# Optimization experiments

Measured on AMD Instinct MI355X. Metric: run time of the kernel, lower is better.

The kernel has to match this reference:

```python
import jax, jax.numpy as jnp
import numpy as np

EPS = 1e-12

def _l2norm(v):
    # torch.nn.functional.normalize(p=2) with eps clamp
    return v / jnp.maximum(jnp.linalg.norm(v), EPS)

def _spectral_weight(W, U):
    # W: (out, in) flattened 1x1 conv weight; U: (1, out) power-iteration buffer.
    # One power iteration, all under stop_gradient (torch.no_grad in original).
    V = _l2norm(U @ W)            # (1, in)
    Unew = _l2norm(V @ W.T)       # (1, out)
    sigma = (Unew @ W @ V.T)[0, 0]
    return W / jax.lax.stop_gradient(sigma)

def _conv1x1(x, W, b):
    # x: (b,c,h,w), W: (o,c), b: (o,)
    return jnp.einsum('oc,bchw->bohw', W, x) + b[None, :, None, None]

def setup_inputs() -> dict:
    key = jax.random.key(0)
    ks = jax.random.split(key, 11)
    B, C, H, W = 4, 256, 64, 64
    Ck = C // 8
    return {
        'x':   jax.random.normal(ks[0], (B, C, H, W), jnp.float32),
        'f_w': jax.random.normal(ks[1], (Ck, C), jnp.float32) * 0.05,
        'f_b': jax.random.normal(ks[2], (Ck,), jnp.float32) * 0.05,
        'f_u': jax.random.uniform(ks[3], (1, Ck), jnp.float32),
        'g_w': jax.random.normal(ks[4], (Ck, C), jnp.float32) * 0.05,
        'g_b': jax.random.normal(ks[5], (Ck,), jnp.float32) * 0.05,
        'g_u': jax.random.uniform(ks[6], (1, Ck), jnp.float32),
        'h_w': jax.random.normal(ks[7], (C, C), jnp.float32) * 0.05,
        'h_b': jax.random.normal(ks[8], (C,), jnp.float32) * 0.05,
        'h_u': jax.random.uniform(ks[9], (1, C), jnp.float32),
        'gamma': jax.random.normal(ks[10], (1, 1), jnp.float32),
    }

def reference(x, f_w, f_b, f_u, g_w, g_b, g_u, h_w, h_b, h_u, gamma):
    b, c, h, w = x.shape
    hw = h * w
    key_ = _conv1x1(x, _spectral_weight(f_w, f_u), f_b).reshape(b, -1, hw).transpose(0, 2, 1)  # (b,hw,ck)
    query = _conv1x1(x, _spectral_weight(g_w, g_u), g_b).reshape(b, -1, hw)                    # (b,ck,hw)
    attn = jax.nn.softmax(jnp.einsum('bnd,bdm->bnm', key_, query), axis=-1)                    # (b,hw,hw)
    value = _conv1x1(x, _spectral_weight(h_w, h_u), h_b).reshape(b, -1, hw)                    # (b,c,hw)
    out = jnp.einsum('bnm,bcm->bnc', attn, value)                                              # (b,hw,c)
    # Faithful to original: raw view of (b,hw,c) contiguous buffer into (b,c,h,w)
    out = out.reshape(b, c, h, w)
    return gamma[0, 0] * out + x
```

## Files before the change

kernel.cpp:

```cpp
#include <hip/hip_runtime.h>


constexpr int kC   = 256;
constexpr int kHW  = 4096;
constexpr int kB   = 4;
constexpr int kCHW = kC * kHW;

typedef short bf16x8 __attribute__((ext_vector_type(8)));
typedef float f32x4  __attribute__((ext_vector_type(4)));
typedef unsigned short u16;

#if __has_builtin(__builtin_amdgcn_exp2f)
#define EXP2(x) __builtin_amdgcn_exp2f(x)
#else
#define EXP2(x) exp2f(x)
#endif

__device__ __forceinline__ u16 f2bf(float f) {
    union { float f; unsigned u; } v; v.f = f;
    unsigned u = v.u;
    return (u16)((u + 0x7fffu + ((u >> 16) & 1u)) >> 16);
}
__device__ __forceinline__ float bf2f(u16 h) {
    union { unsigned u; float f; } v; v.u = ((unsigned)h) << 16;
    return v.f;
}

__global__ __launch_bounds__(1024) void k_sigma(
    const float* __restrict__ fw, const float* __restrict__ fu,
    const float* __restrict__ gw, const float* __restrict__ gu,
    const float* __restrict__ hww, const float* __restrict__ hu,
    float* __restrict__ sig, u16* __restrict__ wh, u16* __restrict__ wl)
{
    const int which = blockIdx.x;
    const float* W = which == 0 ? fw : (which == 1 ? gw : hww);
    const float* U = which == 0 ? fu : (which == 1 ? gu : hu);
    const int O = (which == 2) ? 256 : 32;
    const int t = threadIdx.x;

    __shared__ float par[4][256];
    __shared__ float red[256];
    __shared__ __align__(16) float Vv[256];

    {
        const int i = t & 255, och = t >> 8;
        int olim = O - och * 64; olim = olim < 0 ? 0 : (olim > 64 ? 64 : olim);
        float p = 0.f;
        for (int oo = 0; oo < olim; ++oo) {
            const int o = och * 64 + oo;
            p += U[o] * W[o * 256 + i];
        }
        par[och][i] = p;
    }
    __syncthreads();
    float t1 = 0.f;
    if (t < 256) {
        t1 = par[0][t] + par[1][t] + par[2][t] + par[3][t];
        red[t] = t1 * t1;
    }
    __syncthreads();
    for (int s = 128; s > 0; s >>= 1) { if (t < s) red[t] += red[t + s]; __syncthreads(); }
    if (t < 256) Vv[t] = t1 / fmaxf(sqrtf(red[0]), 1e-12f);
    __syncthreads();

    {
        const int o = t & 255, ich = t >> 8;
        float q = 0.f;
        if (o < O) {
            const float4* Wr = (const float4*)(W + (size_t)o * 256 + ich * 64);
            const float4* Vr = (const float4*)(&Vv[ich * 64]);
#pragma unroll
            for (int j = 0; j < 16; ++j) {
                const float4 w = Wr[j]; const float4 v = Vr[j];
                q += w.x * v.x + w.y * v.y + w.z * v.z + w.w * v.w;
            }
        }
        par[ich][o] = q;
    }
    __syncthreads();
    if (t < 256) {
        const float t2 = par[0][t] + par[1][t] + par[2][t] + par[3][t];
        red[t] = t2 * t2;
    }
    __syncthreads();
    for (int s = 128; s > 0; s >>= 1) { if (t < s) red[t] += red[t + s]; __syncthreads(); }
    if (t == 0) {
        const float s2 = red[0];
        sig[which] = fmaxf(sqrtf(s2), 1e-12f) / s2;
    }

    const int nElem = O * 256;
    const int gbase = (which == 0) ? 0 : (which == 1 ? 32 : 64);
    for (int i = t; i < nElem; i += 1024) {
        const int o = i >> 8, ci = i & 255;
        const int g = gbase + o;
        const int idx = ((g >> 4) * 8 + (ci >> 5)) * 512 + (g & 15) * 32 + (ci & 31);
        const float f = W[i];
        const u16 h = f2bf(f);
        wh[idx] = h;
        wl[idx] = f2bf(f - bf2f(h));
    }
}

__global__ __launch_bounds__(512) void k_proj(
    const float* __restrict__ x,
    const u16* __restrict__ wh, const u16* __restrict__ wl,
    const float* __restrict__ fb, const float* __restrict__ gb,
    const float* __restrict__ hb, const float* __restrict__ sig,
    u16* __restrict__ Kc, u16* __restrict__ Qc, u16* __restrict__ Vb)
{
    __shared__ __align__(16) float xs[256][64];
    __shared__ float bLDS[320];

    const int t = threadIdx.x;
    const int wave = t >> 6, lane = t & 63;
    const int quad = lane >> 4, l15 = lane & 15;
    const int b = blockIdx.y;
    const int n0 = blockIdx.x * 64;
    const int nch = wave & 3, cohalf = wave >> 2;

    constexpr float kLog2e = 1.44269504f;

    {
        const int r4i = lane >> 4, c16 = lane & 15;
        const float* xg = x + (size_t)b * kCHW + (size_t)r4i * kHW + n0 + c16 * 4;
#pragma unroll
        for (int j = 0; j < 8; ++j) {
            const int cibase = (wave * 8 + j) * 4;
            __builtin_amdgcn_global_load_lds(
                (const __attribute__((address_space(1))) void*)(xg + (size_t)cibase * kHW),
                (__attribute__((address_space(3))) void*)&xs[cibase][0], 16, 0, 0);
        }
    }
    if (t < 320) bLDS[t] = (t < 32) ? fb[t]
                         : (t < 64) ? gb[t - 32] * kLog2e
                         : hb[t - 64];
    __syncthreads();

    const int n = nch * 16 + l15;
    bf16x8 bh[8], bl[8];
#pragma unroll
    for (int s = 0; s < 8; ++s) {
        union { u16 a[8]; bf16x8 v; } H, L;
#pragma unroll
        for (int j = 0; j < 8; ++j) {
            const float v = xs[s * 32 + quad * 8 + j][n];
            const u16 h = f2bf(v);
            H.a[j] = h; L.a[j] = f2bf(v - bf2f(h));
        }
        bh[s] = H.v; bl[s] = L.v;
    }

    const u16* whp = wh + l15 * 32 + quad * 8;
    const u16* wlp = wl + l15 * 32 + quad * 8;

    f32x4 acc[10] = {};
#pragma unroll
    for (int c = 0; c < 10; ++c) {
        const size_t base = (size_t)(cohalf * 10 + c) * 4096;
#pragma unroll
        for (int s = 0; s < 8; ++s) {
            const bf16x8 ah = *(const bf16x8*)(whp + base + s * 512);
            const bf16x8 al = *(const bf16x8*)(wlp + base + s * 512);
            acc[c] = __builtin_amdgcn_mfma_f32_16x16x32_bf16(ah, bh[s], acc[c], 0, 0, 0);
            acc[c] = __builtin_amdgcn_mfma_f32_16x16x32_bf16(ah, bl[s], acc[c], 0, 0, 0);
            acc[c] = __builtin_amdgcn_mfma_f32_16x16x32_bf16(al, bh[s], acc[c], 0, 0, 0);
        }
    }

    const float s0 = sig[0], s1 = sig[1] * kLog2e, s2 = sig[2];
#pragma unroll
    for (int c = 0; c < 10; ++c) {
        const int cog0 = (cohalf * 10 + c) * 16;
        const float inv = (cog0 < 32) ? s0 : (cog0 < 64) ? s1 : s2;
#pragma unroll
        for (int r = 0; r < 4; ++r) {
            const int co = cog0 + quad * 4 + r;
            const float v = acc[c][r] * inv + bLDS[co];
            if (co < 64) {
                u16* H = (co < 32) ? Kc : Qc;
                const int d = co & 31;
                const u16 h = f2bf(v);
                const u16 l = f2bf(v - bf2f(h));
                const size_t off = (size_t)(b * kHW + n0 + n) * 64;
                H[off + d] = h;
                H[off + 32 + d] = l;
            } else {
                Vb[((size_t)b * kC + (co - 64)) * kHW + n0 + n] = f2bf(v);
            }
        }
    }
}

__global__ __launch_bounds__(512, 4) void k_attn(
    const u16* __restrict__ Kc, const u16* __restrict__ Qc,
    const u16* __restrict__ Vb,
    u16* __restrict__ Op, float* __restrict__ Sl)
{
    __shared__ __align__(16) u16 Qt[2][4096];
    __shared__ __align__(16) u16 Pt[2][4096];
    __shared__ float lsum[8][16];

    const int t = threadIdx.x;
    const int wave = t >> 6, lane = t & 63;
    const int quad = lane >> 4, l15 = lane & 15;
    const int sg = wave >> 1, half = wave & 1;

    const int id = blockIdx.x;
    const int xcd = id & 7;
    const int b = xcd >> 1;
    const int nb0 = ((xcd & 1) * 32 + ((id >> 3) & 31)) * 64;
    const int mh = id >> 8;
    const int mt0 = mh * 32, mt1 = mt0 + 32;

    const u16* Kb  = Kc + (size_t)b * kHW * 64;
    const u16* Qb  = Qc + (size_t)b * kHW * 64;
    const u16* Vbb = Vb + (size_t)b * kC * kHW;

    const size_t krow = (size_t)(nb0 + sg * 16 + l15) * 64 + (size_t)quad * 8;
    const bf16x8 kh = *(const bf16x8*)(Kb + krow);
    const bf16x8 kl = *(const bf16x8*)(Kb + krow + 32);

    const u16* vrow[2];
#pragma unroll
    for (int ct = 0; ct < 2; ++ct)
        vrow[ct] = Vbb + (size_t)(wave * 32 + ct * 16 + l15) * kHW + quad * 8;

    const int qs_row = lane >> 3, qs_ch = lane & 7;
    const int rloc = wave * 8 + qs_row;
    const int qswz = (qs_ch ^ (rloc & 7)) << 3;

    f32x4 O[8] = {};
    float lrow = 0.f;
    bf16x8 vc[4], vn[4];

    __builtin_amdgcn_global_load_lds(
        (const __attribute__((address_space(1))) void*)
            (Qb + (size_t)(mt0 * 64 + rloc) * 64 + qswz),
        (__attribute__((address_space(3))) void*)&Qt[0][wave * 512], 16, 0, 0);
#pragma unroll
    for (int ct = 0; ct < 2; ++ct)
#pragma unroll
        for (int ks = 0; ks < 2; ++ks)
            vc[ct * 2 + ks] = *(const bf16x8*)(vrow[ct] + mt0 * 64 + ks * 32);
    __syncthreads();

    for (int mt = mt0; mt < mt1; ++mt) {
        const int cur = mt & 1;
        const int m0 = mt * 64;

        if (mt < mt1 - 1) {
            __builtin_amdgcn_global_load_lds(
                (const __attribute__((address_space(1))) void*)
                    (Qb + (size_t)(m0 + 64 + rloc) * 64 + qswz),
                (__attribute__((address_space(3))) void*)&Qt[cur ^ 1][wave * 512], 16, 0, 0);
        }
        const int m0v = (mt < mt1 - 1) ? m0 + 64 : m0;
#pragma unroll
        for (int ct = 0; ct < 2; ++ct)
#pragma unroll
            for (int ks = 0; ks < 2; ++ks)
                vn[ct * 2 + ks] = *(const bf16x8*)(vrow[ct] + m0v + ks * 32);

        f32x4 s[2];
#pragma unroll
        for (int mi2 = 0; mi2 < 2; ++mi2) {
            const int mi = half * 2 + mi2;
            const int rbase = (mi * 16 + l15) * 64;
            const bf16x8 qhv = *(const bf16x8*)&Qt[cur][rbase + ((quad       ^ (l15 & 7)) << 3)];
            const bf16x8 qlv = *(const bf16x8*)&Qt[cur][rbase + (((quad + 4) ^ (l15 & 7)) << 3)];
            f32x4 a = { 0.f, 0.f, 0.f, 0.f };
            a = __builtin_amdgcn_mfma_f32_16x16x32_bf16(qhv, kl, a, 0, 0, 0);
            a = __builtin_amdgcn_mfma_f32_16x16x32_bf16(qlv, kh, a, 0, 0, 0);
            a = __builtin_amdgcn_mfma_f32_16x16x32_bf16(qhv, kh, a, 0, 0, 0);
            s[mi2] = a;
        }

        {
            const int prow = sg * 16 + l15;
#pragma unroll
            for (int mi2 = 0; mi2 < 2; ++mi2) {
                const float p0 = EXP2(s[mi2][0]);
                const float p1 = EXP2(s[mi2][1]);
                const float p2 = EXP2(s[mi2][2]);
                const float p3 = EXP2(s[mi2][3]);
                lrow += (p0 + p1) + (p2 + p3);
                const unsigned d0 = __builtin_amdgcn_perm(
                    __float_as_uint(p1), __float_as_uint(p0), 0x07060302u);
                const unsigned d1 = __builtin_amdgcn_perm(
                    __float_as_uint(p3), __float_as_uint(p2), 0x07060302u);
                const int mi = half * 2 + mi2;
                const int chunk = 2 * mi + (quad >> 1);
                const int off = prow * 64 + ((chunk ^ (l15 & 7)) << 3) + (quad & 1) * 4;
                *(uint2*)(Pt[cur] + off) = make_uint2(d0, d1);
            }
        }

        __syncthreads();

#pragma unroll
        for (int ks = 0; ks < 2; ++ks) {
#pragma unroll
            for (int rg = 0; rg < 4; ++rg) {
                const bf16x8 pa = *(const bf16x8*)&Pt[cur][(rg * 16 + l15) * 64
                                     + (((ks * 4 + quad) ^ (l15 & 7)) << 3)];
#pragma unroll
                for (int ct = 0; ct < 2; ++ct)
                    O[rg * 2 + ct] = __builtin_amdgcn_mfma_f32_16x16x32_bf16(
                        pa, vc[ct * 2 + ks], O[rg * 2 + ct], 0, 0, 0);
            }
        }

#pragma unroll
        for (int i = 0; i < 4; ++i) vc[i] = vn[i];
    }

    lrow += __shfl_xor(lrow, 16);
    lrow += __shfl_xor(lrow, 32);
    if (lane < 16) lsum[wave][l15] = lrow;
    __syncthreads();
    if (half == 0 && lane < 16)
        Sl[(size_t)(mh * 4 + b) * kHW + nb0 + sg * 16 + l15]
            = lsum[wave][l15] + lsum[wave ^ 1][l15];

    u16* Opb = Op + (size_t)(mh * 4 + b) * kHW * 256;
#pragma unroll
    for (int rg = 0; rg < 4; ++rg) {
#pragma unroll
        for (int ct = 0; ct < 2; ++ct) {
#pragma unroll
            for (int r = 0; r < 4; ++r) {
                const int nn = nb0 + rg * 16 + quad * 4 + r;
                const int c = wave * 32 + ct * 16 + l15;
                Opb[(size_t)nn * 256 + c] = f2bf(O[rg * 2 + ct][r]);
            }
        }
    }
}

__global__ __launch_bounds__(256) void k_merge(
    const float* __restrict__ x, const float* __restrict__ gamma,
    const u16* __restrict__ Op, const float* __restrict__ Sl,
    float* __restrict__ out)
{
    const int tid = blockIdx.x * 256 + threadIdx.x;
    const int cg = tid & 31;
    const int n  = (tid >> 5) & 4095;
    const int b  = tid >> 17;
    const int c0 = cg * 8;

    const float la = Sl[(size_t)b * kHW + n];
    const float lb = Sl[(size_t)(4 + b) * kHW + n];
    const float invL = 1.f / (la + lb);
    const float g = gamma[0];

    const size_t base = ((size_t)b * kHW + n) * 256 + c0;
    const uint4 A = *(const uint4*)(Op + base);
    const uint4 B = *(const uint4*)(Op + base + (size_t)4 * kHW * 256);
    const float4 x0 = *(const float4*)(x + base);
    const float4 x1 = *(const float4*)(x + base + 4);

    float o[8];
    const unsigned aw[4] = { A.x, A.y, A.z, A.w };
    const unsigned bw[4] = { B.x, B.y, B.z, B.w };
#pragma unroll
    for (int j = 0; j < 8; ++j) {
        const float va = bf2f((u16)(aw[j >> 1] >> ((j & 1) * 16)));
        const float vb = bf2f((u16)(bw[j >> 1] >> ((j & 1) * 16)));
        o[j] = (va + vb) * invL;
    }
    float4 r0, r1;
    r0.x = g * o[0] + x0.x; r0.y = g * o[1] + x0.y;
    r0.z = g * o[2] + x0.z; r0.w = g * o[3] + x0.w;
    r1.x = g * o[4] + x1.x; r1.y = g * o[5] + x1.y;
    r1.z = g * o[6] + x1.z; r1.w = g * o[7] + x1.w;
    *(float4*)(out + base)     = r0;
    *(float4*)(out + base + 4) = r1;
}

extern "C" void kernel_launch(void* const* d_in, const int* in_sizes, int n_in,
                              void* d_out, int out_size, void* d_ws, size_t ws_size,
                              hipStream_t stream)
{
    const float* x     = (const float*)d_in[0];
    const float* fw    = (const float*)d_in[1];
    const float* fb    = (const float*)d_in[2];
    const float* fu    = (const float*)d_in[3];
    const float* gw    = (const float*)d_in[4];
    const float* gb    = (const float*)d_in[5];
    const float* gu    = (const float*)d_in[6];
    const float* hww   = (const float*)d_in[7];
    const float* hb    = (const float*)d_in[8];
    const float* hu    = (const float*)d_in[9];
    const float* gamma = (const float*)d_in[10];
    float* out = (float*)d_out;

    char* ws = (char*)d_ws;
    float* sig = (float*)ws;
    u16* wh = (u16*)(ws + 1024);
    u16* wl = wh + 320 * 256;
    u16* Kc = (u16*)(ws + (1u << 20));
    u16* Qc = (u16*)(ws + (3u << 20));
    u16* Vb = (u16*)(ws + (5u << 20));
    u16* Op = (u16*)(ws + (16u << 20));
    float* Sl = (float*)(ws + (32u << 20));

    k_sigma<<<dim3(3), dim3(1024), 0, stream>>>(fw, fu, gw, gu, hww, hu, sig, wh, wl);
    k_proj<<<dim3(64, 4), dim3(512), 0, stream>>>(x, wh, wl, fb, gb, hb, sig,
                                                  Kc, Qc, Vb);
    k_attn<<<dim3(512), dim3(512), 0, stream>>>(Kc, Qc, Vb, Op, Sl);
    k_merge<<<dim3(2048), dim3(256), 0, stream>>>(x, gamma, Op, Sl, out);
}
```

Baseline: 245.4 us.

## Split attention key range into four partitions when workspace allows

Makes the number of split-K partitions along the attention m dimension a runtime parameter. When the workspace is large enough it uses 4 partitions, giving 1024 blocks instead of 512, and the merge kernel becomes templated to sum 4 partial outputs and row sums. It also raises the launch_bounds occupancy hint from 4 to 8 and repacks the workspace offsets. The cost is more partial-output traffic (4x 8MB bf16) in the merge pass and possible register pressure from the tighter launch bound.

```diff
diff --git a/kernel.cpp b/kernel.cpp
--- a/kernel.cpp
+++ b/kernel.cpp
@@ -192,10 +192,10 @@
     }
 }
 
-__global__ __launch_bounds__(512, 4) void k_attn(
+__global__ __launch_bounds__(512, 8) void k_attn(
     const u16* __restrict__ Kc, const u16* __restrict__ Qc,
     const u16* __restrict__ Vb,
-    u16* __restrict__ Op, float* __restrict__ Sl)
+    u16* __restrict__ Op, float* __restrict__ Sl, int mtiles)
 {
     __shared__ __align__(16) u16 Qt[2][4096];
     __shared__ __align__(16) u16 Pt[2][4096];
@@ -211,7 +211,7 @@
     const int b = xcd >> 1;
     const int nb0 = ((xcd & 1) * 32 + ((id >> 3) & 31)) * 64;
     const int mh = id >> 8;
-    const int mt0 = mh * 32, mt1 = mt0 + 32;
+    const int mt0 = mh * mtiles, mt1 = mt0 + mtiles;
 
     const u16* Kb  = Kc + (size_t)b * kHW * 64;
     const u16* Qb  = Qc + (size_t)b * kHW * 64;
@@ -338,6 +338,7 @@
     }
 }
 
+template <int NS>
 __global__ __launch_bounds__(256) void k_merge(
     const float* __restrict__ x, const float* __restrict__ gamma,
     const u16* __restrict__ Op, const float* __restrict__ Sl,
@@ -349,31 +350,31 @@
     const int b  = tid >> 17;
     const int c0 = cg * 8;
 
-    const float la = Sl[(size_t)b * kHW + n];
-    const float lb = Sl[(size_t)(4 + b) * kHW + n];
-    const float invL = 1.f / (la + lb);
+    float l = 0.f;
+#pragma unroll
+    for (int s = 0; s < NS; ++s) l += Sl[(size_t)(s * 4 + b) * kHW + n];
+    const float invL = 1.f / l;
     const float g = gamma[0];
 
     const size_t base = ((size_t)b * kHW + n) * 256 + c0;
-    const uint4 A = *(const uint4*)(Op + base);
-    const uint4 B = *(const uint4*)(Op + base + (size_t)4 * kHW * 256);
+
+    float o[8] = {};
+#pragma unroll
+    for (int s = 0; s < NS; ++s) {
+        const uint4 A = *(const uint4*)(Op + base + (size_t)s * 4 * kHW * 256);
+        const unsigned aw[4] = { A.x, A.y, A.z, A.w };
+#pragma unroll
+        for (int j = 0; j < 8; ++j)
+            o[j] += bf2f((u16)(aw[j >> 1] >> ((j & 1) * 16)));
+    }
+
     const float4 x0 = *(const float4*)(x + base);
     const float4 x1 = *(const float4*)(x + base + 4);
-
-    float o[8];
-    const unsigned aw[4] = { A.x, A.y, A.z, A.w };
-    const unsigned bw[4] = { B.x, B.y, B.z, B.w };
-#pragma unroll
-    for (int j = 0; j < 8; ++j) {
-        const float va = bf2f((u16)(aw[j >> 1] >> ((j & 1) * 16)));
-        const float vb = bf2f((u16)(bw[j >> 1] >> ((j & 1) * 16)));
-        o[j] = (va + vb) * invL;
-    }
     float4 r0, r1;
-    r0.x = g * o[0] + x0.x; r0.y = g * o[1] + x0.y;
-    r0.z = g * o[2] + x0.z; r0.w = g * o[3] + x0.w;
-    r1.x = g * o[4] + x1.x; r1.y = g * o[5] + x1.y;
-    r1.z = g * o[6] + x1.z; r1.w = g * o[7] + x1.w;
+    r0.x = g * o[0] * invL + x0.x; r0.y = g * o[1] * invL + x0.y;
+    r0.z = g * o[2] * invL + x0.z; r0.w = g * o[3] * invL + x0.w;
+    r1.x = g * o[4] * invL + x1.x; r1.y = g * o[5] * invL + x1.y;
+    r1.z = g * o[6] * invL + x1.z; r1.w = g * o[7] * invL + x1.w;
     *(float4*)(out + base)     = r0;
     *(float4*)(out + base + 4) = r1;
 }
@@ -399,15 +400,24 @@
     float* sig = (float*)ws;
     u16* wh = (u16*)(ws + 1024);
     u16* wl = wh + 320 * 256;
-    u16* Kc = (u16*)(ws + (1u << 20));
-    u16* Qc = (u16*)(ws + (3u << 20));
-    u16* Vb = (u16*)(ws + (5u << 20));
-    u16* Op = (u16*)(ws + (16u << 20));
-    float* Sl = (float*)(ws + (32u << 20));
+    u16* Kc = (u16*)(ws + (512u << 10));
+    u16* Qc = (u16*)(ws + (2560u << 10));
+    u16* Vb = (u16*)(ws + (4608u << 10));
+    char* opBase = ws + (12800u << 10);
+
+    const size_t need4 = (12800u << 10) + 4ull * 8 * 1024 * 1024 + (256u << 10);
+    const int ns = (ws_size >= need4) ? 4 : 2;
+    const int mtiles = 64 / ns;
+
+    u16* Op = (u16*)opBase;
+    float* Sl = (float*)(opBase + (size_t)ns * 8 * 1024 * 1024);
 
     k_sigma<<<dim3(3), dim3(1024), 0, stream>>>(fw, fu, gw, gu, hww, hu, sig, wh, wl);
     k_proj<<<dim3(64, 4), dim3(512), 0, stream>>>(x, wh, wl, fb, gb, hb, sig,
                                                   Kc, Qc, Vb);
-    k_attn<<<dim3(512), dim3(512), 0, stream>>>(Kc, Qc, Vb, Op, Sl);
-    k_merge<<<dim3(2048), dim3(256), 0, stream>>>(x, gamma, Op, Sl, out);
-}
+    k_attn<<<dim3(256 * ns), dim3(512), 0, stream>>>(Kc, Qc, Vb, Op, Sl, mtiles);
+    if (ns == 4)
+        k_merge<4><<<dim3(2048), dim3(256), 0, stream>>>(x, gamma, Op, Sl, out);
+    else
+        k_merge<2><<<dim3(2048), dim3(256), 0, stream>>>(x, gamma, Op, Sl, out);
+}
```

New measurement: 702.1 us. 186% more time.

## Drop V register prefetch, raise wave priority around MFMA, specialize sigma loops

Applied to the files above, without the earlier changes.

The attention loop stops double-buffering V fragments in registers one tile ahead and loads the current tile's V at the top of each iteration. This frees registers but exposes global load latency. Wave priority is raised with s_setprio around the QK and PV MFMA blocks so matrix work from different waves interleaves better with memory work. The spectral-norm kernel's U·W loop is also specialized with fixed trip counts and unrolling, which is a minor cost.

```diff
diff --git a/kernel.cpp b/kernel.cpp
--- a/kernel.cpp
+++ b/kernel.cpp
@@ -44,11 +44,18 @@
 
     {
         const int i = t & 255, och = t >> 8;
-        int olim = O - och * 64; olim = olim < 0 ? 0 : (olim > 64 ? 64 : olim);
         float p = 0.f;
-        for (int oo = 0; oo < olim; ++oo) {
-            const int o = och * 64 + oo;
-            p += U[o] * W[o * 256 + i];
+        if (O == 256) {
+            const float* Wc = W + (size_t)(och * 64) * 256 + i;
+            const float* Uc = U + och * 64;
+#pragma unroll 8
+            for (int oo = 0; oo < 64; ++oo)
+                p += Uc[oo] * Wc[(size_t)oo * 256];
+        } else if (och == 0) {
+            const float* Wc = W + i;
+#pragma unroll 8
+            for (int oo = 0; oo < 32; ++oo)
+                p += U[oo] * Wc[(size_t)oo * 256];
         }
         par[och][i] = p;
     }
@@ -232,17 +239,12 @@
 
     f32x4 O[8] = {};
     float lrow = 0.f;
-    bf16x8 vc[4], vn[4];
+    bf16x8 vc[4];
 
     __builtin_amdgcn_global_load_lds(
         (const __attribute__((address_space(1))) void*)
             (Qb + (size_t)(mt0 * 64 + rloc) * 64 + qswz),
         (__attribute__((address_space(3))) void*)&Qt[0][wave * 512], 16, 0, 0);
-#pragma unroll
-    for (int ct = 0; ct < 2; ++ct)
-#pragma unroll
-        for (int ks = 0; ks < 2; ++ks)
-            vc[ct * 2 + ks] = *(const bf16x8*)(vrow[ct] + mt0 * 64 + ks * 32);
     __syncthreads();
 
     for (int mt = mt0; mt < mt1; ++mt) {
@@ -255,14 +257,14 @@
                     (Qb + (size_t)(m0 + 64 + rloc) * 64 + qswz),
                 (__attribute__((address_space(3))) void*)&Qt[cur ^ 1][wave * 512], 16, 0, 0);
         }
-        const int m0v = (mt < mt1 - 1) ? m0 + 64 : m0;
 #pragma unroll
         for (int ct = 0; ct < 2; ++ct)
 #pragma unroll
             for (int ks = 0; ks < 2; ++ks)
-                vn[ct * 2 + ks] = *(const bf16x8*)(vrow[ct] + m0v + ks * 32);
+                vc[ct * 2 + ks] = *(const bf16x8*)(vrow[ct] + m0 + ks * 32);
 
         f32x4 s[2];
+        __builtin_amdgcn_s_setprio(1);
 #pragma unroll
         for (int mi2 = 0; mi2 < 2; ++mi2) {
             const int mi = half * 2 + mi2;
@@ -275,6 +277,7 @@
             a = __builtin_amdgcn_mfma_f32_16x16x32_bf16(qhv, kh, a, 0, 0, 0);
             s[mi2] = a;
         }
+        __builtin_amdgcn_s_setprio(0);
 
         {
             const int prow = sg * 16 + l15;
@@ -298,6 +301,7 @@
 
         __syncthreads();
 
+        __builtin_amdgcn_s_setprio(1);
 #pragma unroll
         for (int ks = 0; ks < 2; ++ks) {
 #pragma unroll
@@ -310,9 +314,7 @@
                         pa, vc[ct * 2 + ks], O[rg * 2 + ct], 0, 0, 0);
             }
         }
-
-#pragma unroll
-        for (int i = 0; i < 4; ++i) vc[i] = vn[i];
+        __builtin_amdgcn_s_setprio(0);
     }
 
     lrow += __shfl_xor(lrow, 16);
```

New measurement: 231.3 us. 5.8% less time.
